# Optimization experiments

Hardware: AMD Instinct MI355X
Metric: run time of the kernel (lower is better)

Reference implementation:

```python
import jax, jax.numpy as jnp
import numpy as np

NEG_BIG = -9e15


def gat_layer(h, adj, W, a, alpha, concat):
    # h: (N, Fin), W: (Fin, Fout), a: (2*Fout, 1)
    Wh = h @ W                                   # (N, Fout)
    F = Wh.shape[1]
    # e[i,j] = LeakyReLU(cat(Wh_i, Wh_j) @ a) = LeakyReLU(s_i + d_j)
    s = Wh @ a[:F, 0]                            # (N,)
    d = Wh @ a[F:, 0]                            # (N,)
    e = jax.nn.leaky_relu(s[:, None] + d[None, :], negative_slope=alpha)  # (N, N)
    e = jnp.where(adj > 0, e, NEG_BIG)
    att = jax.nn.softmax(e, axis=1)              # (N, N)
    out = att @ Wh                               # (N, Fout)
    return jax.nn.elu(out) if concat else out


def setup_inputs() -> dict:
    key = jax.random.key(0)
    ks = jax.random.split(key, 12)
    N, nfeat, nhid, nlatent, nclass = 8192, 512, 256, 64, 16

    def xavier(k, shape):
        gain = 1.414
        fan_in, fan_out = shape[0], shape[1]
        bound = gain * np.sqrt(6.0 / (fan_in + fan_out))
        return jax.random.uniform(k, shape, jnp.float32, -bound, bound)

    x = jax.random.normal(ks[0], (N, nfeat), jnp.float32)
    adj = jax.random.randint(ks[1], (N, N), 0, 2, jnp.int32)
    eps = jax.random.normal(ks[2], (N, nlatent), jnp.float32)
    return {
        "x": x,
        "adj": adj,
        "eps": eps,
        "W1": xavier(ks[3], (nfeat, nhid)),
        "a1": xavier(ks[4], (2 * nhid, 1)),
        "Wmu": xavier(ks[5], (nhid, nlatent)),
        "amu": xavier(ks[6], (2 * nlatent, 1)),
        "Wlv": xavier(ks[7], (nhid, nlatent)),
        "alv": xavier(ks[8], (2 * nlatent, 1)),
        "Wc": xavier(ks[9], (nlatent, nclass)),
        "bc": jnp.zeros((nclass,), jnp.float32),
    }


def reference(x, adj, eps, W1, a1, Wmu, amu, Wlv, alv, Wc, bc):
    alpha = 0.2  # LeakyReLU negative slope
    # eval mode: all dropouts are identity
    h = gat_layer(x, adj, W1, a1, alpha, concat=True)      # (N, nhid)
    mu = gat_layer(h, adj, Wmu, amu, alpha, concat=False)  # (N, nlatent)
    logvar = gat_layer(h, adj, Wlv, alv, alpha, concat=False)
    z = mu + eps * jnp.exp(0.5 * logvar)
    logits = z @ Wc + bc                                   # (N, nclass)
    return logits, mu, logvar
```

## Files before the change

### kernel.cpp

```cpp
#include <hip/hip_runtime.h>

typedef unsigned short u16;
typedef __attribute__((ext_vector_type(8))) short short8;
typedef __attribute__((ext_vector_type(4))) float f32x4;

#define NROW 8192

__device__ __forceinline__ float bf2f(u16 h) {
  unsigned u = ((unsigned)h) << 16;
  return __builtin_bit_cast(float, u);
}
__device__ __forceinline__ float ldf(const void* p, size_t i, int f32) {
  return f32 ? ((const float*)p)[i] : bf2f(((const u16*)p)[i]);
}
__device__ __forceinline__ u16 f2bf(float f) {
  unsigned b = __builtin_bit_cast(unsigned, f);
  b += 0x7FFFu + ((b >> 16) & 1u);
  return (u16)(b >> 16);
}

__global__ void detect3(const u16* __restrict__ xr, unsigned* __restrict__ mode) {
  __shared__ int zc, bg;
  int t = threadIdx.x;
  if (t == 0) { zc = 0; bg = 0; }
  __syncthreads();
  int zeros_even = 0; int big = 0;
  for (int i = t; i < 4096; i += 256) {
    u16 v = xr[i];
    if (!(i & 1) && v == 0) zeros_even++;
    if (fabsf(bf2f(v)) > 1e6f) big = 1;
  }
  atomicAdd(&zc, zeros_even);
  if (big) atomicOr(&bg, 1);
  __syncthreads();
  if (t == 0) *mode = (zc > 512 || bg) ? 1u : 0u;
}

__global__ void detect_adj(const unsigned* __restrict__ a, unsigned* __restrict__ amode) {
  __shared__ int clo;
  int t = threadIdx.x;
  if (t == 0) clo = 0;
  __syncthreads();
  int c = 0;
  for (int i = t; i < 4096; i += 256)
    if (a[i] == 0x00003F80u) c++;
  atomicAdd(&clo, c);
  __syncthreads();
  if (t == 0) *amode = (clo > 32) ? 1u : 0u;
}

struct AdjRaw { int4 w0, w1; };
__device__ __forceinline__ AdjRaw adj_load(const void* adj, size_t base, int amode) {
  AdjRaw r;
  if (amode == 0) {
    const int4* p = (const int4*)((const int*)adj + base);
    r.w0 = p[0]; r.w1 = p[1];
  } else {
    r.w0 = *(const int4*)((const u16*)adj + base);
    r.w1 = make_int4(0, 0, 0, 0);
  }
  return r;
}
__device__ __forceinline__ void adj_decode(const AdjRaw& r, int amode, int* aa) {
  if (amode == 0) {
    aa[0] = r.w0.x != 0; aa[1] = r.w0.y != 0; aa[2] = r.w0.z != 0; aa[3] = r.w0.w != 0;
    aa[4] = r.w1.x != 0; aa[5] = r.w1.y != 0; aa[6] = r.w1.z != 0; aa[7] = r.w1.w != 0;
  } else {
    aa[0] = (r.w0.x & 0xFFFF) != 0; aa[1] = ((unsigned)r.w0.x >> 16) != 0;
    aa[2] = (r.w0.y & 0xFFFF) != 0; aa[3] = ((unsigned)r.w0.y >> 16) != 0;
    aa[4] = (r.w0.z & 0xFFFF) != 0; aa[5] = ((unsigned)r.w0.z >> 16) != 0;
    aa[6] = (r.w0.w & 0xFFFF) != 0; aa[7] = ((unsigned)r.w0.w >> 16) != 0;
  }
}

__global__ __launch_bounds__(256) void gemm_mfma(const u16* __restrict__ Abf,
    const u16* __restrict__ BT, float* __restrict__ C, int K, int N) {
  int tid = threadIdx.x;
  int l = tid & 63, w = tid >> 6;
  int m0 = blockIdx.y * 64, n0 = blockIdx.x * 64;
  const u16* arow = Abf + (size_t)(m0 + w * 16 + (l & 15)) * K + (l >> 4) * 8;
  const u16* brow = BT + (size_t)(n0 + (l & 15)) * K + (l >> 4) * 8;
  f32x4 acc[4];
#pragma unroll
  for (int nt = 0; nt < 4; ++nt) acc[nt] = (f32x4){0.f, 0.f, 0.f, 0.f};
  for (int k0 = 0; k0 < K; k0 += 32) {
    short8 a = *(const short8*)(arow + k0);
#pragma unroll
    for (int nt = 0; nt < 4; ++nt) {
      short8 b = *(const short8*)(brow + (size_t)nt * 16 * K + k0);
      acc[nt] = __builtin_amdgcn_mfma_f32_16x16x32_bf16(a, b, acc[nt], 0, 0, 0);
    }
  }
#pragma unroll
  for (int nt = 0; nt < 4; ++nt)
#pragma unroll
    for (int q = 0; q < 4; ++q)
      C[(size_t)(m0 + w * 16 + (l >> 4) * 4 + q) * N + n0 + nt * 16 + (l & 15)] =
          acc[nt][q];
}

__global__ __launch_bounds__(256) void gemm2_dual(const u16* __restrict__ Abf,
    const u16* __restrict__ BT0, const u16* __restrict__ BT1,
    float* __restrict__ C0, float* __restrict__ C1) {
  const int K = 256, N = 64;
  const u16* BT = blockIdx.x ? BT1 : BT0;
  float* C = blockIdx.x ? C1 : C0;
  int tid = threadIdx.x, l = tid & 63, w = tid >> 6;
  int m0 = blockIdx.y * 64;
  const u16* arow = Abf + (size_t)(m0 + w * 16 + (l & 15)) * K + (l >> 4) * 8;
  const u16* brow = BT + (size_t)(l & 15) * K + (l >> 4) * 8;
  f32x4 acc[4];
#pragma unroll
  for (int nt = 0; nt < 4; ++nt) acc[nt] = (f32x4){0.f, 0.f, 0.f, 0.f};
  for (int k0 = 0; k0 < K; k0 += 32) {
    short8 a = *(const short8*)(arow + k0);
#pragma unroll
    for (int nt = 0; nt < 4; ++nt) {
      short8 b = *(const short8*)(brow + (size_t)nt * 16 * K + k0);
      acc[nt] = __builtin_amdgcn_mfma_f32_16x16x32_bf16(a, b, acc[nt], 0, 0, 0);
    }
  }
#pragma unroll
  for (int nt = 0; nt < 4; ++nt)
#pragma unroll
    for (int q = 0; q < 4; ++q)
      C[(size_t)(m0 + w * 16 + (l >> 4) * 4 + q) * N + nt * 16 + (l & 15)] = acc[nt][q];
}

__global__ __launch_bounds__(256) void convert_bf16(const void* __restrict__ in,
    u16* __restrict__ out, int n8, const unsigned* __restrict__ modep) {
  int f32 = (int)*modep;
  int i = blockIdx.x * 256 + threadIdx.x;
  if (i >= n8) return;
  if (f32) {
    float4 v0 = ((const float4*)in)[(size_t)i * 2];
    float4 v1 = ((const float4*)in)[(size_t)i * 2 + 1];
    ushort4 o0 = {f2bf(v0.x), f2bf(v0.y), f2bf(v0.z), f2bf(v0.w)};
    ushort4 o1 = {f2bf(v1.x), f2bf(v1.y), f2bf(v1.z), f2bf(v1.w)};
    ((ushort4*)out)[(size_t)i * 2] = o0;
    ((ushort4*)out)[(size_t)i * 2 + 1] = o1;
  } else {
    ((int4*)out)[i] = ((const int4*)in)[i];
  }
}

__global__ __launch_bounds__(256) void transpose_bf16(const float* __restrict__ in,
    u16* __restrict__ out, int M, int F) {
  __shared__ float t[32][33];
  int m0 = blockIdx.x * 32, f0 = blockIdx.y * 32;
  int c = threadIdx.x & 31, r = threadIdx.x >> 5;
  for (int rr = r; rr < 32; rr += 8)
    t[rr][c] = in[(size_t)(m0 + rr) * F + f0 + c];
  __syncthreads();
  for (int rr = r; rr < 32; rr += 8)
    out[(size_t)(f0 + rr) * M + m0 + c] = f2bf(t[c][rr]);
}

__global__ __launch_bounds__(256) void transpose_pair(const float* __restrict__ in0,
    const float* __restrict__ in1, u16* __restrict__ out0, u16* __restrict__ out1,
    int M, int F) {
  const float* in = blockIdx.z ? in1 : in0;
  u16* out = blockIdx.z ? out1 : out0;
  __shared__ float t[32][33];
  int m0 = blockIdx.x * 32, f0 = blockIdx.y * 32;
  int c = threadIdx.x & 31, r = threadIdx.x >> 5;
  for (int rr = r; rr < 32; rr += 8)
    t[rr][c] = in[(size_t)(m0 + rr) * F + f0 + c];
  __syncthreads();
  for (int rr = r; rr < 32; rr += 8)
    out[(size_t)(f0 + rr) * M + m0 + c] = f2bf(t[c][rr]);
}

__global__ __launch_bounds__(256) void transpose_any(const void* __restrict__ in,
    u16* __restrict__ out, int M, int F, const unsigned* __restrict__ modep) {
  int f32 = (int)*modep;
  __shared__ u16 t[32][33];
  int m0 = blockIdx.x * 32, f0 = blockIdx.y * 32;
  int c = threadIdx.x & 31, r = threadIdx.x >> 5;
  for (int rr = r; rr < 32; rr += 8)
    t[rr][c] = f2bf(ldf(in, (size_t)(m0 + rr) * F + f0 + c, f32));
  __syncthreads();
  for (int rr = r; rr < 32; rr += 8)
    out[(size_t)(f0 + rr) * M + m0 + c] = t[c][rr];
}

__global__ __launch_bounds__(256) void transpose_w2(const void* __restrict__ in0,
    const void* __restrict__ in1, u16* __restrict__ out0, u16* __restrict__ out1,
    int M, int F, const unsigned* __restrict__ modep) {
  int f32 = (int)*modep;
  const void* in = blockIdx.z ? in1 : in0;
  u16* out = blockIdx.z ? out1 : out0;
  __shared__ u16 t[32][33];
  int m0 = blockIdx.x * 32, f0 = blockIdx.y * 32;
  int c = threadIdx.x & 31, r = threadIdx.x >> 5;
  for (int rr = r; rr < 32; rr += 8)
    t[rr][c] = f2bf(ldf(in, (size_t)(m0 + rr) * F + f0 + c, f32));
  __syncthreads();
  for (int rr = r; rr < 32; rr += 8)
    out[(size_t)(f0 + rr) * M + m0 + c] = t[c][rr];
}

__global__ __launch_bounds__(256) void sd_f32(const float* __restrict__ Wh,
    const void* __restrict__ a2, float* __restrict__ s, float* __restrict__ d,
    int F, const unsigned* __restrict__ modep) {
  int f32 = (int)*modep;
  int row = blockIdx.x * 4 + (threadIdx.x >> 6);
  int l = threadIdx.x & 63;
  float ss = 0.f, dd = 0.f;
  for (int k = l; k < F; k += 64) {
    float wv = Wh[(size_t)row * F + k];
    ss += wv * ldf(a2, k, f32);
    dd += wv * ldf(a2, F + k, f32);
  }
#pragma unroll
  for (int off = 32; off > 0; off >>= 1) {
    ss += __shfl_down(ss, off, 64);
    dd += __shfl_down(dd, off, 64);
  }
  if (l == 0) { s[row] = ss; d[row] = dd; }
}

__global__ __launch_bounds__(256) void sd_dual(const float* __restrict__ Wh0,
    const float* __restrict__ Wh1, const void* __restrict__ a0,
    const void* __restrict__ a1, float* __restrict__ s0, float* __restrict__ s1,
    float* __restrict__ d0, float* __restrict__ d1,
    const unsigned* __restrict__ modep) {
  int f32 = (int)*modep;
  int L = blockIdx.y;
  const float* Wh = L ? Wh1 : Wh0;
  const void* a2 = L ? a1 : a0;
  int row = blockIdx.x * 4 + (threadIdx.x >> 6);
  int l = threadIdx.x & 63;
  float wv = Wh[(size_t)row * 64 + l];
  float ss = wv * ldf(a2, l, f32);
  float dd = wv * ldf(a2, 64 + l, f32);
#pragma unroll
  for (int off = 32; off > 0; off >>= 1) {
    ss += __shfl_down(ss, off, 64);
    dd += __shfl_down(dd, off, 64);
  }
  if (l == 0) { (L ? s1 : s0)[row] = ss; (L ? d1 : d0)[row] = dd; }
}

__global__ __launch_bounds__(256) void dmax_reduce(const float* __restrict__ da,
    const float* __restrict__ db, float* __restrict__ cells) {
  const float* d = blockIdx.x ? db : da;
  __shared__ float red[256];
  float m = -3.4e38f;
  for (int i = threadIdx.x; i < NROW; i += 256) m = fmaxf(m, d[i]);
  red[threadIdx.x] = m;
  __syncthreads();
#pragma unroll
  for (int sft = 128; sft > 0; sft >>= 1) {
    if (threadIdx.x < sft) red[threadIdx.x] = fmaxf(red[threadIdx.x], red[threadIdx.x + sft]);
    __syncthreads();
  }
  if (threadIdx.x == 0) cells[blockIdx.x * 16] = red[0];
}

__device__ __forceinline__ int pa_off(int L, int ks, int mh, int row, int kg) {
  return ((L * 8 + ks * 2 + mh) << 10) + (row << 6) + ((kg ^ ((row >> 1) & 3)) << 4);
}

template <int NL>
__global__ __launch_bounds__(512) void flash_mfma(
    const u16* __restrict__ whTa, const u16* __restrict__ whTb,
    const float* __restrict__ sa, const float* __restrict__ da,
    const float* __restrict__ sb, const float* __restrict__ db,
    const float* __restrict__ cella, const float* __restrict__ cellb,
    const void* __restrict__ adj, const unsigned* __restrict__ amodep,
    void* __restrict__ o0, void* __restrict__ o1,
    void* __restrict__ o2, void* __restrict__ o3) {
  constexpr int NIT = NROW / 128;
  constexpr int NTW = (NL == 1) ? 2 : 1;
  constexpr int FDIM = (NL == 1) ? 256 : 64;
  __shared__ __align__(16) char PA[2][NL * 8192];
  __shared__ __align__(16) float dd_[NL][NROW];
  __shared__ float sv_[NL][32], Ms_[NL][32], ls_[NL][32];
  int tid = threadIdx.x;
  int amode = (int)*amodep;
  int r0 = blockIdx.x * 32;
  if (tid < 32 * NL) {
    int L = tid >> 5, i = tid & 31;
    float Dm = L ? *cellb : *cella;
    float t0 = (L ? sb : sa)[r0 + i];
    sv_[L][i] = t0;
    float m = t0 + Dm;
    Ms_[L][i] = fmaxf(m, 0.2f * m);
  }
  for (int u = tid; u < NL * (NROW / 4); u += 512) {
    int L = u / (NROW / 4), uu = u - L * (NROW / 4);
    ((float4*)dd_[L])[uu] = ((const float4*)(L ? db : da))[uu];
  }
  __syncthreads();
  int sr = tid >> 4, sjo = tid & 15;
  int ks_w = sjo >> 2, kg_w = sjo & 3, mh_w = sr >> 4, row_w = sr & 15;
  int l = tid & 63, w = tid >> 6;
  int layer = (NL == 1) ? 0 : (w >> 2);
  int ntb = (NL == 1) ? (w * 2) : (w & 3);
  const u16* whT = layer ? whTb : whTa;
  f32x4 acc[2][NTW];
#pragma unroll
  for (int m = 0; m < 2; ++m)
#pragma unroll
    for (int n = 0; n < NTW; ++n) acc[m][n] = (f32x4){0.f, 0.f, 0.f, 0.f};
  float psum[NL];
#pragma unroll
  for (int L = 0; L < NL; ++L) psum[L] = 0.f;
  size_t abase = (size_t)(r0 + sr) * NROW + sjo * 8;

  AdjRaw adjA = adj_load(adj, abase, amode);
  AdjRaw adjB = adj_load(adj, abase + 128, amode);
  for (int it = 0; it < NIT; ++it) {
    int j0 = it * 128;
    int cur = it & 1;
    short8 bfr[4][NTW];
#pragma unroll
    for (int ks = 0; ks < 4; ++ks) {
      size_t jcol = (size_t)(j0 + ks * 32 + (l >> 4) * 8);
#pragma unroll
      for (int nt = 0; nt < NTW; ++nt)
        bfr[ks][nt] =
            *(const short8*)&whT[(size_t)((ntb + nt) * 16 + (l & 15)) * NROW + jcol];
    }
    AdjRaw adjN = adjB;
    if (it + 2 < NIT) adjN = adj_load(adj, abase + (size_t)(it + 2) * 128, amode);
    int aa[8];
    adj_decode(adjA, amode, aa);
    char* pab = PA[cur];
#pragma unroll
    for (int L = 0; L < NL; ++L) {
      float sv = sv_[L][sr], Mr = Ms_[L][sr];
      float4 dv0 = *(const float4*)&dd_[L][j0 + sjo * 8];
      float4 dv1 = *(const float4*)&dd_[L][j0 + sjo * 8 + 4];
      float dvv[8] = {dv0.x, dv0.y, dv0.z, dv0.w, dv1.x, dv1.y, dv1.z, dv1.w};
      short8 pk;
      float ps = 0.f;
#pragma unroll
      for (int q = 0; q < 8; ++q) {
        float t = sv + dvv[q];
        float e = fmaxf(t, 0.2f * t) - Mr;
        float p = aa[q] ? __expf(e) : 0.f;
        ps += p;
        pk[q] = (short)f2bf(p);
      }
      psum[L] += ps;
      *(short8*)(pab + pa_off(L, ks_w, mh_w, row_w, kg_w)) = pk;
    }
    asm volatile("s_waitcnt lgkmcnt(0)" ::: "memory");
    __builtin_amdgcn_s_barrier();
    __builtin_amdgcn_sched_barrier(0);
    __builtin_amdgcn_s_setprio(1);
#pragma unroll
    for (int ks = 0; ks < 4; ++ks) {
      short8 a0 = *(const short8*)(pab + pa_off(layer, ks, 0, l & 15, l >> 4));
      short8 a1 = *(const short8*)(pab + pa_off(layer, ks, 1, l & 15, l >> 4));
#pragma unroll
      for (int nt = 0; nt < NTW; ++nt) {
        acc[0][nt] = __builtin_amdgcn_mfma_f32_16x16x32_bf16(a0, bfr[ks][nt],
                                                             acc[0][nt], 0, 0, 0);
        acc[1][nt] = __builtin_amdgcn_mfma_f32_16x16x32_bf16(a1, bfr[ks][nt],
                                                             acc[1][nt], 0, 0, 0);
      }
    }
    __builtin_amdgcn_s_setprio(0);
    adjA = adjB; adjB = adjN;
  }
  __syncthreads();
  float* red = (float*)PA;
#pragma unroll
  for (int L = 0; L < NL; ++L) red[L * 512 + tid] = psum[L];
  __syncthreads();
  if (tid < 32 * NL) {
    int L = tid >> 5, r = tid & 31;
    float t = 0.f;
#pragma unroll
    for (int q = 0; q < 16; ++q) t += red[L * 512 + r * 16 + q];
    ls_[L][r] = t;
  }
  __syncthreads();
  if constexpr (NL == 1) {
    u16* hb = (u16*)o0;
#pragma unroll
    for (int m = 0; m < 2; ++m)
#pragma unroll
      for (int nt = 0; nt < NTW; ++nt)
#pragma unroll
        for (int q = 0; q < 4; ++q) {
          int r = m * 16 + (l >> 4) * 4 + q;
          int c = (ntb + nt) * 16 + (l & 15);
          float x = acc[m][nt][q] / ls_[0][r];
          x = (x > 0.f) ? x : (__expf(x) - 1.f);
          hb[(size_t)(r0 + r) * FDIM + c] = f2bf(x);
        }
  } else {
    float* of = (float*)(layer ? o2 : o0);
    float* od = (float*)(layer ? o3 : o1);
#pragma unroll
    for (int m = 0; m < 2; ++m)
#pragma unroll
      for (int q = 0; q < 4; ++q) {
        int r = m * 16 + (l >> 4) * 4 + q;
        int c = ntb * 16 + (l & 15);
        float x = acc[m][0][q] / ls_[layer][r];
        size_t idx = (size_t)(r0 + r) * FDIM + c;
        of[idx] = x;
        od[idx] = x;
      }
  }
}

__global__ __launch_bounds__(256) void logits_f32(const float* __restrict__ mu,
    const float* __restrict__ lv, const void* __restrict__ eps,
    const void* __restrict__ Wc, const void* __restrict__ bcv,
    float* __restrict__ outL, const unsigned* __restrict__ modep) {
  int f32 = (int)*modep;
  __shared__ float zs[64 * 64];
  __shared__ float wcs[64 * 16];
  int tid = threadIdx.x;
  for (int i = tid; i < 1024; i += 256) wcs[i] = ldf(Wc, i, f32);
  int rl = tid >> 2, cs = (tid & 3) * 16;
  int row = blockIdx.x * 64 + rl;
  size_t rb64 = (size_t)row * 64;
  for (int c = cs; c < cs + 16; ++c)
    zs[rl * 64 + c] = mu[rb64 + c] + ldf(eps, rb64 + c, f32) * __expf(0.5f * lv[rb64 + c]);
  __syncthreads();
  for (int it = tid; it < 1024; it += 256) {
    int r = it >> 4, oc = it & 15;
    float a = ldf(bcv, oc, f32);
    for (int c = 0; c < 64; ++c) a += zs[r * 64 + c] * wcs[c * 16 + oc];
    outL[(size_t)(blockIdx.x * 64 + r) * 16 + oc] = a;
  }
}

extern "C" void kernel_launch(void* const* d_in, const int* in_sizes, int n_in,
                              void* d_out, int out_size, void* d_ws, size_t ws_size,
                              hipStream_t stream) {
  (void)out_size; (void)ws_size;
  int ix = 0, iadj = 1, ieps = 2, iW1 = 3, ia1 = 4, iWmu = 5, iamu = 6,
      iWlv = 7, ialv = 8, iWc = 9, ibc = 10;
  {
    int fmu = -1, flv = -1, fam = -1, fal = -1;
    for (int i = 0; i < n_in; ++i) {
      switch (in_sizes[i]) {
        case 67108864: iadj = i; break;
        case 4194304:  ix   = i; break;
        case 524288:   ieps = i; break;
        case 131072:   iW1  = i; break;
        case 512:      ia1  = i; break;
        case 1024:     iWc  = i; break;
        case 16:       ibc  = i; break;
        case 16384:    if (fmu < 0) fmu = i; else flv = i; break;
        case 128:      if (fam < 0) fam = i; else fal = i; break;
        default: break;
      }
    }
    if (fmu >= 0 && flv >= 0) { iWmu = fmu; iWlv = flv; }
    if (fam >= 0 && fal >= 0) { iamu = fam; ialv = fal; }
  }
  const void* adj = d_in[iadj];
  char* ws = (char*)d_ws;
  const size_t KB = 1024, MB = 1024 * 1024;
  float* wh1   = (float*)(ws + 0);
  float* whmu  = (float*)(ws + 0);
  float* whlv  = (float*)(ws + 2 * MB);
  float* muf   = (float*)(ws + 4 * MB);
  float* lvf   = (float*)(ws + 6 * MB);
  u16*   xbf   = (u16*)(ws + 8 * MB);
  u16*   whT1  = (u16*)(ws + 8 * MB);
  u16*   hbf   = (u16*)(ws + 12 * MB);
  u16*   whmuT = (u16*)(ws + 20 * MB);
  u16*   whlvT = (u16*)(ws + 21 * MB);
  u16*   W1T   = (u16*)(ws + 22 * MB);
  u16*   WmuT  = (u16*)(ws + 22 * MB + 256 * KB);
  u16*   WlvT  = (u16*)(ws + 22 * MB + 288 * KB);
  float* s1    = (float*)(ws + 24 * MB + 96 * KB);
  float* d1    = (float*)(ws + 24 * MB + 128 * KB);
  float* smu   = (float*)(ws + 24 * MB + 160 * KB);
  float* dmu   = (float*)(ws + 24 * MB + 192 * KB);
  float* slv   = (float*)(ws + 24 * MB + 224 * KB);
  float* dlv   = (float*)(ws + 24 * MB + 256 * KB);
  float* dmaxv = (float*)(ws + 24 * MB + 288 * KB);
  unsigned* mode  = (unsigned*)(ws + 24 * MB + 289 * KB);
  unsigned* amode = (unsigned*)(ws + 24 * MB + 290 * KB);

  float* out_logits = (float*)d_out;
  float* out_mu     = (float*)d_out + 131072;
  float* out_lv     = (float*)d_out + 655360;

  detect3<<<1, 256, 0, stream>>>((const u16*)d_in[ix], mode);
  detect_adj<<<1, 256, 0, stream>>>((const unsigned*)adj, amode);

  convert_bf16<<<2048, 256, 0, stream>>>(d_in[ix], xbf, 524288, mode);
  transpose_any<<<dim3(16, 8), 256, 0, stream>>>(d_in[iW1], W1T, 512, 256, mode);
  gemm_mfma<<<dim3(4, 128), 256, 0, stream>>>(xbf, W1T, wh1, 512, 256);
  transpose_bf16<<<dim3(256, 8), 256, 0, stream>>>(wh1, whT1, 8192, 256);
  sd_f32<<<2048, 256, 0, stream>>>(wh1, d_in[ia1], s1, d1, 256, mode);
  dmax_reduce<<<1, 256, 0, stream>>>(d1, d1, dmaxv + 0);
  flash_mfma<1><<<256, 512, 0, stream>>>(whT1, nullptr, s1, d1,
      nullptr, nullptr, dmaxv + 0, nullptr, adj, amode,
      hbf, nullptr, nullptr, nullptr);

  transpose_w2<<<dim3(8, 2, 2), 256, 0, stream>>>(d_in[iWmu], d_in[iWlv],
      WmuT, WlvT, 256, 64, mode);
  gemm2_dual<<<dim3(2, 128), 256, 0, stream>>>(hbf, WmuT, WlvT, whmu, whlv);
  transpose_pair<<<dim3(256, 2, 2), 256, 0, stream>>>(whmu, whlv, whmuT, whlvT,
      8192, 64);
  sd_dual<<<dim3(2048, 2), 256, 0, stream>>>(whmu, whlv, d_in[iamu], d_in[ialv],
      smu, slv, dmu, dlv, mode);
  dmax_reduce<<<2, 256, 0, stream>>>(dmu, dlv, dmaxv + 16);
  flash_mfma<2><<<256, 512, 0, stream>>>(whmuT, whlvT, smu, dmu, slv, dlv,
      dmaxv + 16, dmaxv + 32, adj, amode,
      muf, out_mu, lvf, out_lv);

  logits_f32<<<128, 256, 0, stream>>>(muf, lvf, d_in[ieps], d_in[iWc], d_in[ibc], out_logits, mode);
}
```

Measured before the change: 616.8 us.

## Pack adjacency into bitmask once and widen flash kernel to 1024 threads

Adds a pre-pass that compresses the int32 (or bf16) adjacency matrix into one bit per edge. Both flash attention passes then read 8 MB of bits instead of re-reading the 256 MB int matrix each time. The flash kernel also doubles to 1024 threads with 256-column tiles, and each wave now owns one 16-row half, which changes the MFMA work split and doubles the LDS staging buffer. The logits kernel is re-gridded to 32 rows per block. The extra bit-packing pass still has to read the full adjacency once.

```diff
diff --git a/kernel.cpp b/kernel.cpp
--- a/kernel.cpp
+++ b/kernel.cpp
@@ -49,27 +49,24 @@
   if (t == 0) *amode = (clo > 32) ? 1u : 0u;
 }
 
-struct AdjRaw { int4 w0, w1; };
-__device__ __forceinline__ AdjRaw adj_load(const void* adj, size_t base, int amode) {
-  AdjRaw r;
-  if (amode == 0) {
-    const int4* p = (const int4*)((const int*)adj + base);
-    r.w0 = p[0]; r.w1 = p[1];
-  } else {
-    r.w0 = *(const int4*)((const u16*)adj + base);
-    r.w1 = make_int4(0, 0, 0, 0);
-  }
-  return r;
-}
-__device__ __forceinline__ void adj_decode(const AdjRaw& r, int amode, int* aa) {
-  if (amode == 0) {
-    aa[0] = r.w0.x != 0; aa[1] = r.w0.y != 0; aa[2] = r.w0.z != 0; aa[3] = r.w0.w != 0;
-    aa[4] = r.w1.x != 0; aa[5] = r.w1.y != 0; aa[6] = r.w1.z != 0; aa[7] = r.w1.w != 0;
-  } else {
-    aa[0] = (r.w0.x & 0xFFFF) != 0; aa[1] = ((unsigned)r.w0.x >> 16) != 0;
-    aa[2] = (r.w0.y & 0xFFFF) != 0; aa[3] = ((unsigned)r.w0.y >> 16) != 0;
-    aa[4] = (r.w0.z & 0xFFFF) != 0; aa[5] = ((unsigned)r.w0.z >> 16) != 0;
-    aa[6] = (r.w0.w & 0xFFFF) != 0; aa[7] = ((unsigned)r.w0.w >> 16) != 0;
+__global__ __launch_bounds__(256) void adj_bits(const void* __restrict__ adj,
+    unsigned char* __restrict__ bits, const unsigned* __restrict__ amodep) {
+  int amode = (int)*amodep;
+  for (size_t b = (size_t)blockIdx.x * 256 + threadIdx.x; b < 8388608; b += 524288) {
+    size_t e0 = b * 8;
+    unsigned byte = 0;
+    if (amode == 0) {
+      int4 a0 = *(const int4*)((const int*)adj + e0);
+      int4 a1 = *(const int4*)((const int*)adj + e0 + 4);
+      byte = (a0.x != 0) | ((a0.y != 0) << 1) | ((a0.z != 0) << 2) | ((a0.w != 0) << 3) |
+             ((a1.x != 0) << 4) | ((a1.y != 0) << 5) | ((a1.z != 0) << 6) | ((a1.w != 0) << 7);
+    } else {
+      ushort4 a0 = *(const ushort4*)((const u16*)adj + e0);
+      ushort4 a1 = *(const ushort4*)((const u16*)adj + e0 + 4);
+      byte = (a0.x != 0) | ((a0.y != 0) << 1) | ((a0.z != 0) << 2) | ((a0.w != 0) << 3) |
+             ((a1.x != 0) << 4) | ((a1.y != 0) << 5) | ((a1.z != 0) << 6) | ((a1.w != 0) << 7);
+    }
+    bits[b] = (unsigned char)byte;
   }
 }
 
@@ -259,26 +256,25 @@
 }
 
 __device__ __forceinline__ int pa_off(int L, int ks, int mh, int row, int kg) {
-  return ((L * 8 + ks * 2 + mh) << 10) + (row << 6) + ((kg ^ ((row >> 1) & 3)) << 4);
+  return ((L * 16 + ks * 2 + mh) << 10) + (row << 6) + ((kg ^ ((row >> 1) & 3)) << 4);
 }
 
 template <int NL>
-__global__ __launch_bounds__(512) void flash_mfma(
+__global__ __launch_bounds__(1024) void flash_mfma(
     const u16* __restrict__ whTa, const u16* __restrict__ whTb,
     const float* __restrict__ sa, const float* __restrict__ da,
     const float* __restrict__ sb, const float* __restrict__ db,
     const float* __restrict__ cella, const float* __restrict__ cellb,
-    const void* __restrict__ adj, const unsigned* __restrict__ amodep,
+    const unsigned char* __restrict__ abits,
     void* __restrict__ o0, void* __restrict__ o1,
     void* __restrict__ o2, void* __restrict__ o3) {
-  constexpr int NIT = NROW / 128;
+  constexpr int NIT = NROW / 256;
   constexpr int NTW = (NL == 1) ? 2 : 1;
   constexpr int FDIM = (NL == 1) ? 256 : 64;
-  __shared__ __align__(16) char PA[2][NL * 8192];
+  __shared__ __align__(16) char PA[2][NL * 16384];
   __shared__ __align__(16) float dd_[NL][NROW];
   __shared__ float sv_[NL][32], Ms_[NL][32], ls_[NL][32];
   int tid = threadIdx.x;
-  int amode = (int)*amodep;
   int r0 = blockIdx.x * 32;
   if (tid < 32 * NL) {
     int L = tid >> 5, i = tid & 31;
@@ -288,45 +284,42 @@
     float m = t0 + Dm;
     Ms_[L][i] = fmaxf(m, 0.2f * m);
   }
-  for (int u = tid; u < NL * (NROW / 4); u += 512) {
+  for (int u = tid; u < NL * (NROW / 4); u += 1024) {
     int L = u / (NROW / 4), uu = u - L * (NROW / 4);
     ((float4*)dd_[L])[uu] = ((const float4*)(L ? db : da))[uu];
   }
   __syncthreads();
-  int sr = tid >> 4, sjo = tid & 15;
+  int sr = tid >> 5, sjo = tid & 31;
   int ks_w = sjo >> 2, kg_w = sjo & 3, mh_w = sr >> 4, row_w = sr & 15;
   int l = tid & 63, w = tid >> 6;
-  int layer = (NL == 1) ? 0 : (w >> 2);
-  int ntb = (NL == 1) ? (w * 2) : (w & 3);
+  int layer = (NL == 1) ? 0 : (w >> 3);
+  int mh_p  = (NL == 1) ? (w >> 3) : ((w >> 2) & 1);
+  int ntb   = (NL == 1) ? ((w & 7) * 2) : (w & 3);
   const u16* whT = layer ? whTb : whTa;
-  f32x4 acc[2][NTW];
-#pragma unroll
-  for (int m = 0; m < 2; ++m)
-#pragma unroll
-    for (int n = 0; n < NTW; ++n) acc[m][n] = (f32x4){0.f, 0.f, 0.f, 0.f};
+  f32x4 acc[NTW];
+#pragma unroll
+  for (int n = 0; n < NTW; ++n) acc[n] = (f32x4){0.f, 0.f, 0.f, 0.f};
   float psum[NL];
 #pragma unroll
   for (int L = 0; L < NL; ++L) psum[L] = 0.f;
-  size_t abase = (size_t)(r0 + sr) * NROW + sjo * 8;
-
-  AdjRaw adjA = adj_load(adj, abase, amode);
-  AdjRaw adjB = adj_load(adj, abase + 128, amode);
+  int bofs = (r0 + sr) * 1024 + sjo;
+
+  unsigned char abA = abits[bofs];
+  unsigned char abB = abits[bofs + 32];
   for (int it = 0; it < NIT; ++it) {
-    int j0 = it * 128;
+    int j0 = it * 256;
     int cur = it & 1;
-    short8 bfr[4][NTW];
-#pragma unroll
-    for (int ks = 0; ks < 4; ++ks) {
+    short8 bfr[8][NTW];
+#pragma unroll
+    for (int ks = 0; ks < 8; ++ks) {
       size_t jcol = (size_t)(j0 + ks * 32 + (l >> 4) * 8);
 #pragma unroll
       for (int nt = 0; nt < NTW; ++nt)
         bfr[ks][nt] =
             *(const short8*)&whT[(size_t)((ntb + nt) * 16 + (l & 15)) * NROW + jcol];
     }
-    AdjRaw adjN = adjB;
-    if (it + 2 < NIT) adjN = adj_load(adj, abase + (size_t)(it + 2) * 128, amode);
-    int aa[8];
-    adj_decode(adjA, amode, aa);
+    unsigned char abN = abB;
+    if (it + 2 < NIT) abN = abits[bofs + (it + 2) * 32];
     char* pab = PA[cur];
 #pragma unroll
     for (int L = 0; L < NL; ++L) {
@@ -340,7 +333,7 @@
       for (int q = 0; q < 8; ++q) {
         float t = sv + dvv[q];
         float e = fmaxf(t, 0.2f * t) - Mr;
-        float p = aa[q] ? __expf(e) : 0.f;
+        float p = ((abA >> q) & 1) ? __expf(e) : 0.f;
         ps += p;
         pk[q] = (short)f2bf(p);
       }
@@ -352,61 +345,53 @@
     __builtin_amdgcn_sched_barrier(0);
     __builtin_amdgcn_s_setprio(1);
 #pragma unroll
-    for (int ks = 0; ks < 4; ++ks) {
-      short8 a0 = *(const short8*)(pab + pa_off(layer, ks, 0, l & 15, l >> 4));
-      short8 a1 = *(const short8*)(pab + pa_off(layer, ks, 1, l & 15, l >> 4));
-#pragma unroll
-      for (int nt = 0; nt < NTW; ++nt) {
-        acc[0][nt] = __builtin_amdgcn_mfma_f32_16x16x32_bf16(a0, bfr[ks][nt],
-                                                             acc[0][nt], 0, 0, 0);
-        acc[1][nt] = __builtin_amdgcn_mfma_f32_16x16x32_bf16(a1, bfr[ks][nt],
-                                                             acc[1][nt], 0, 0, 0);
-      }
+    for (int ks = 0; ks < 8; ++ks) {
+      short8 a = *(const short8*)(pab + pa_off(layer, ks, mh_p, l & 15, l >> 4));
+#pragma unroll
+      for (int nt = 0; nt < NTW; ++nt)
+        acc[nt] = __builtin_amdgcn_mfma_f32_16x16x32_bf16(a, bfr[ks][nt],
+                                                          acc[nt], 0, 0, 0);
     }
     __builtin_amdgcn_s_setprio(0);
-    adjA = adjB; adjB = adjN;
+    abA = abB; abB = abN;
   }
   __syncthreads();
   float* red = (float*)PA;
 #pragma unroll
-  for (int L = 0; L < NL; ++L) red[L * 512 + tid] = psum[L];
+  for (int L = 0; L < NL; ++L) red[L * 1024 + tid] = psum[L];
   __syncthreads();
   if (tid < 32 * NL) {
     int L = tid >> 5, r = tid & 31;
     float t = 0.f;
 #pragma unroll
-    for (int q = 0; q < 16; ++q) t += red[L * 512 + r * 16 + q];
+    for (int q = 0; q < 32; ++q) t += red[L * 1024 + r * 32 + q];
     ls_[L][r] = t;
   }
   __syncthreads();
   if constexpr (NL == 1) {
     u16* hb = (u16*)o0;
 #pragma unroll
-    for (int m = 0; m < 2; ++m)
-#pragma unroll
-      for (int nt = 0; nt < NTW; ++nt)
-#pragma unroll
-        for (int q = 0; q < 4; ++q) {
-          int r = m * 16 + (l >> 4) * 4 + q;
-          int c = (ntb + nt) * 16 + (l & 15);
-          float x = acc[m][nt][q] / ls_[0][r];
-          x = (x > 0.f) ? x : (__expf(x) - 1.f);
-          hb[(size_t)(r0 + r) * FDIM + c] = f2bf(x);
-        }
+    for (int nt = 0; nt < NTW; ++nt)
+#pragma unroll
+      for (int q = 0; q < 4; ++q) {
+        int r = mh_p * 16 + (l >> 4) * 4 + q;
+        int c = (ntb + nt) * 16 + (l & 15);
+        float x = acc[nt][q] / ls_[0][r];
+        x = (x > 0.f) ? x : (__expf(x) - 1.f);
+        hb[(size_t)(r0 + r) * FDIM + c] = f2bf(x);
+      }
   } else {
     float* of = (float*)(layer ? o2 : o0);
     float* od = (float*)(layer ? o3 : o1);
 #pragma unroll
-    for (int m = 0; m < 2; ++m)
-#pragma unroll
-      for (int q = 0; q < 4; ++q) {
-        int r = m * 16 + (l >> 4) * 4 + q;
-        int c = ntb * 16 + (l & 15);
-        float x = acc[m][0][q] / ls_[layer][r];
-        size_t idx = (size_t)(r0 + r) * FDIM + c;
-        of[idx] = x;
-        od[idx] = x;
-      }
+    for (int q = 0; q < 4; ++q) {
+      int r = mh_p * 16 + (l >> 4) * 4 + q;
+      int c = ntb * 16 + (l & 15);
+      float x = acc[0][q] / ls_[layer][r];
+      size_t idx = (size_t)(r0 + r) * FDIM + c;
+      of[idx] = x;
+      od[idx] = x;
+    }
   }
 }
 
@@ -415,21 +400,22 @@
     const void* __restrict__ Wc, const void* __restrict__ bcv,
     float* __restrict__ outL, const unsigned* __restrict__ modep) {
   int f32 = (int)*modep;
-  __shared__ float zs[64 * 64];
+  __shared__ float zs[32 * 64];
   __shared__ float wcs[64 * 16];
   int tid = threadIdx.x;
   for (int i = tid; i < 1024; i += 256) wcs[i] = ldf(Wc, i, f32);
-  int rl = tid >> 2, cs = (tid & 3) * 16;
-  int row = blockIdx.x * 64 + rl;
-  size_t rb64 = (size_t)row * 64;
-  for (int c = cs; c < cs + 16; ++c)
-    zs[rl * 64 + c] = mu[rb64 + c] + ldf(eps, rb64 + c, f32) * __expf(0.5f * lv[rb64 + c]);
-  __syncthreads();
-  for (int it = tid; it < 1024; it += 256) {
+  int row0 = blockIdx.x * 32;
+  for (int i = tid; i < 2048; i += 256) {
+    int r = i >> 6, c = i & 63;
+    size_t g = (size_t)(row0 + r) * 64 + c;
+    zs[i] = mu[g] + ldf(eps, g, f32) * __expf(0.5f * lv[g]);
+  }
+  __syncthreads();
+  for (int it = tid; it < 512; it += 256) {
     int r = it >> 4, oc = it & 15;
     float a = ldf(bcv, oc, f32);
     for (int c = 0; c < 64; ++c) a += zs[r * 64 + c] * wcs[c * 16 + oc];
-    outL[(size_t)(blockIdx.x * 64 + r) * 16 + oc] = a;
+    outL[(size_t)(row0 + r) * 16 + oc] = a;
   }
 }
 
@@ -483,6 +469,7 @@
   float* dmaxv = (float*)(ws + 24 * MB + 288 * KB);
   unsigned* mode  = (unsigned*)(ws + 24 * MB + 289 * KB);
   unsigned* amode = (unsigned*)(ws + 24 * MB + 290 * KB);
+  unsigned char* abits = (unsigned char*)(ws + 25 * MB);
 
   float* out_logits = (float*)d_out;
   float* out_mu     = (float*)d_out + 131072;
@@ -490,6 +477,7 @@
 
   detect3<<<1, 256, 0, stream>>>((const u16*)d_in[ix], mode);
   detect_adj<<<1, 256, 0, stream>>>((const unsigned*)adj, amode);
+  adj_bits<<<2048, 256, 0, stream>>>(adj, abits, amode);
 
   convert_bf16<<<2048, 256, 0, stream>>>(d_in[ix], xbf, 524288, mode);
   transpose_any<<<dim3(16, 8), 256, 0, stream>>>(d_in[iW1], W1T, 512, 256, mode);
@@ -497,8 +485,8 @@
   transpose_bf16<<<dim3(256, 8), 256, 0, stream>>>(wh1, whT1, 8192, 256);
   sd_f32<<<2048, 256, 0, stream>>>(wh1, d_in[ia1], s1, d1, 256, mode);
   dmax_reduce<<<1, 256, 0, stream>>>(d1, d1, dmaxv + 0);
-  flash_mfma<1><<<256, 512, 0, stream>>>(whT1, nullptr, s1, d1,
-      nullptr, nullptr, dmaxv + 0, nullptr, adj, amode,
+  flash_mfma<1><<<256, 1024, 0, stream>>>(whT1, nullptr, s1, d1,
+      nullptr, nullptr, dmaxv + 0, nullptr, abits,
       hbf, nullptr, nullptr, nullptr);
 
   transpose_w2<<<dim3(8, 2, 2), 256, 0, stream>>>(d_in[iWmu], d_in[iWlv],
@@ -509,9 +497,9 @@
   sd_dual<<<dim3(2048, 2), 256, 0, stream>>>(whmu, whlv, d_in[iamu], d_in[ialv],
       smu, slv, dmu, dlv, mode);
   dmax_reduce<<<2, 256, 0, stream>>>(dmu, dlv, dmaxv + 16);
-  flash_mfma<2><<<256, 512, 0, stream>>>(whmuT, whlvT, smu, dmu, slv, dlv,
-      dmaxv + 16, dmaxv + 32, adj, amode,
+  flash_mfma<2><<<256, 1024, 0, stream>>>(whmuT, whlvT, smu, dmu, slv, dlv,
+      dmaxv + 16, dmaxv + 32, abits,
       muf, out_mu, lvf, out_lv);
 
-  logits_f32<<<128, 256, 0, stream>>>(muf, lvf, d_in[ieps], d_in[iWc], d_in[ibc], out_logits, mode);
-}
+  logits_f32<<<256, 256, 0, stream>>>(muf, lvf, d_in[ieps], d_in[iWc], d_in[ibc], out_logits, mode);
+}
```

Result: slower. 851.7 us (+38.1%).
